# Optimization experiments

Hardware: AMD Instinct MI355X
Metric: run time of the kernel (lower is better)

## Reference

```python
import jax, jax.numpy as jnp
import numpy as np

B, T, S, D, V, PAD = 8, 4095, 2048, 300, 32000, 1


def setup_inputs() -> dict:
    key = jax.random.key(0)
    k1, k2, k3, k4 = jax.random.split(key, 4)
    # tokens in [2, V) so none collide with padding_idx
    x = jax.random.randint(k1, (B, T), 2, V, dtype=jnp.int64)
    # first S nodes are leaves: indices (i, i); remaining T-S are internal spans hi > lo
    leaf = jnp.arange(S, dtype=jnp.int64)
    leaf_pairs = jnp.broadcast_to(jnp.stack([leaf, leaf], -1)[None], (B, S, 2))
    n_int = T - S
    lo = jax.random.randint(k2, (B, n_int), 0, S - 1, dtype=jnp.int64)
    span = jax.random.randint(k3, (B, n_int), 1, 64, dtype=jnp.int64)
    hi = jnp.minimum(lo + span, S - 1)
    int_pairs = jnp.stack([lo, hi], -1)
    indices = jnp.concatenate([leaf_pairs, int_pairs], axis=1)  # [B, T, 2]
    W = jax.random.normal(k4, (V, D), jnp.float32) * 0.02
    W = W.at[PAD].set(0.0)  # padding_idx row is zero, as in nn.Embedding
    return {"x": x, "indices": indices, "W": W}


def reference(x, indices, W):
    b, t = x.shape
    s = (t + 1) // 2
    # _retrieve_leaves: left-pack tokens whose (lo==hi) and token != PAD
    is_leaf = (indices[:, :, 0] == indices[:, :, 1]) & (x != PAD)  # [b,t]
    pos = jnp.cumsum(is_leaf.astype(jnp.int32), axis=1) - 1       # packed slot per leaf
    safe_pos = jnp.where(is_leaf, pos, s)                          # out-of-range -> dropped
    leaves = jnp.full((b, s), PAD, dtype=x.dtype)
    leaves = leaves.at[jnp.arange(b)[:, None], safe_pos].set(x, mode="drop")  # [b,s]
    # interval mask: lo <= r <= hi  (computed as (r>=lo) XOR (r>hi), as in source)
    r = jnp.arange(s)[None, None, :]                               # [1,1,s]
    mask = ((r >= indices[:, :, 0:1]) ^ (r > indices[:, :, 1:2])).astype(W.dtype)  # [b,t,s]
    emb = W[leaves]                                                # [b,s,D]
    denom = jnp.maximum(mask.sum(-1, keepdims=True), 1.0)          # [b,t,1]
    # same math as (mask[...,None] * emb[:,None]).sum(2), without the [b,t,s,D] tensor
    out = jnp.einsum("bts,bsd->btd", mask, emb) / denom
    return out
```

## Files before the change

### kernel.cpp

```cpp
#include <hip/hip_runtime.h>


#define BB 8
#define TT 4095
#define SS 2048
#define DD 300
#define D4 75
#define PADIDX 1
#define CHUNK 16
#define NC (SS / CHUNK)
#define NTB 320

typedef float f4 __attribute__((ext_vector_type(4)));

__global__ __launch_bounds__(NTB) void csumP_kernel(const int* __restrict__ x,
                                                    const float* __restrict__ W,
                                                    float* __restrict__ csum,
                                                    float* __restrict__ P,
                                                    float* __restrict__ out) {
    int blk = blockIdx.x;
    int b = blk & 7, c = blk >> 3;
    int tid = threadIdx.x;
    int g = tid / 80, j = tid - g * 80;
    __shared__ f4 sw[CHUNK][D4];
    const int* xb = x + b * TT + c * CHUNK;
    const f4* W4 = (const f4*)W;
    f4* out4 = (f4*)out;
    if (j < D4) {
#pragma unroll
        for (int i = 0; i < 4; ++i) {
            int row = g * 4 + i;
            f4 v = W4[(size_t)xb[row] * D4 + j];
            sw[row][j] = v;
            __builtin_nontemporal_store(
                v, &out4[((size_t)b * TT + c * CHUNK + row) * D4 + j]);
        }
    }
    __syncthreads();
    if (j >= D4) return;

    f4* P4 = (f4*)P + (size_t)b * (SS + 1) * D4;
    f4 run = (f4)0.f;
    for (int k = 0; k < g * 4; ++k) run += sw[k][j];
    int s0 = c * CHUNK;
#pragma unroll
    for (int i = 0; i < 4; ++i) {
        int row = g * 4 + i;
        P4[(size_t)(s0 + row) * D4 + j] = run;
        run += sw[row][j];
    }
    if (g == 3) {
        ((f4*)csum)[(b * NC + c) * D4 + j] = run;
        if (c == NC - 1) P4[(size_t)SS * D4 + j] = (f4)0.f;
    }
}

__global__ __launch_bounds__(128) void base_kernel(const float* __restrict__ csum,
                                                   float* __restrict__ base) {
    int b = blockIdx.x;
    int j = threadIdx.x;
    if (j >= D4) return;
    const f4* csum4 = (const f4*)csum + (size_t)b * NC * D4;
    f4* base4 = (f4*)base + (size_t)b * (NC + 1) * D4;
    f4 run = (f4)0.f;
#pragma unroll 16
    for (int c = 0; c < NC; ++c) {
        base4[c * D4 + j] = run;
        run += csum4[c * D4 + j];
    }
    base4[NC * D4 + j] = run;
}

__global__ __launch_bounds__(NTB) void out_int_kernel(const int* __restrict__ idx,
                                                      const float* __restrict__ P,
                                                      const float* __restrict__ base,
                                                      float* __restrict__ out) {
    int tid = threadIdx.x;
    int r = tid / 80, j = tid - r * 80;
    int b = blockIdx.x & 7;
    int g = blockIdx.x >> 3;
    const f4* P4 = (const f4*)P + (size_t)b * (SS + 1) * D4;
    const f4* B4 = (const f4*)base + (size_t)b * (NC + 1) * D4;
    f4* out4 = (f4*)out;
    const int2* ixb = (const int2*)(idx + 2 * b * TT);
#pragma unroll
    for (int it = 0; it < 4; ++it) {
        int lr = SS + g * 16 + it * 4 + r;
        if (lr >= TT || j >= D4) continue;
        int2 pr = ixb[lr];
        int u = pr.y + 1;
        int a = min(pr.x, u), e = max(pr.x, u);
        a = max(0, min(a, SS));
        e = max(0, min(e, SS));
        int cnt = e - a;
        float inv = 1.0f / (float)(cnt > 0 ? cnt : 1);
        f4 ve = P4[(size_t)e * D4 + j] + B4[(e >> 4) * D4 + j];
        f4 va = P4[(size_t)a * D4 + j] + B4[(a >> 4) * D4 + j];
        f4 o = (ve - va) * inv;
        __builtin_nontemporal_store(o, &out4[((size_t)b * TT + lr) * D4 + j]);
    }
}

extern "C" void kernel_launch(void* const* d_in, const int* in_sizes, int n_in,
                              void* d_out, int out_size, void* d_ws, size_t ws_size,
                              hipStream_t stream) {
    const int* x = (const int*)d_in[0];
    const int* idx = (const int*)d_in[1];
    const float* W = (const float*)d_in[2];
    float* out = (float*)d_out;

    char* ws = (char*)d_ws;
    float* csum = (float*)ws;
    float* base = (float*)(ws + 1228800);
    float* P = (float*)(ws + 1228800 + 1238400);

    csumP_kernel<<<BB * NC, NTB, 0, stream>>>(x, W, csum, P, out);
    base_kernel<<<BB, 128, 0, stream>>>(csum, base);
    out_int_kernel<<<BB * NC, NTB, 0, stream>>>(idx, P, base, out);
}
```

Measured before the change: 111.1 us.

## Drop chunk-prefix kernel; sum chunk totals directly per interval

Removes the serial base_kernel, which scanned 128 chunk sums per batch using only 8 blocks, along with its launch. Each interval thread now adds the per-chunk totals between the lo and hi chunks itself. Spans are under 64, so this is at most about 4 extra loads per output. It trades a serial, low-occupancy kernel and a launch for a few extra scattered loads per output.

```diff
diff --git a/kernel.cpp b/kernel.cpp
--- a/kernel.cpp
+++ b/kernel.cpp
@@ -55,32 +55,16 @@
     }
 }
 
-__global__ __launch_bounds__(128) void base_kernel(const float* __restrict__ csum,
-                                                   float* __restrict__ base) {
-    int b = blockIdx.x;
-    int j = threadIdx.x;
-    if (j >= D4) return;
-    const f4* csum4 = (const f4*)csum + (size_t)b * NC * D4;
-    f4* base4 = (f4*)base + (size_t)b * (NC + 1) * D4;
-    f4 run = (f4)0.f;
-#pragma unroll 16
-    for (int c = 0; c < NC; ++c) {
-        base4[c * D4 + j] = run;
-        run += csum4[c * D4 + j];
-    }
-    base4[NC * D4 + j] = run;
-}
-
 __global__ __launch_bounds__(NTB) void out_int_kernel(const int* __restrict__ idx,
                                                       const float* __restrict__ P,
-                                                      const float* __restrict__ base,
+                                                      const float* __restrict__ csum,
                                                       float* __restrict__ out) {
     int tid = threadIdx.x;
     int r = tid / 80, j = tid - r * 80;
     int b = blockIdx.x & 7;
     int g = blockIdx.x >> 3;
     const f4* P4 = (const f4*)P + (size_t)b * (SS + 1) * D4;
-    const f4* B4 = (const f4*)base + (size_t)b * (NC + 1) * D4;
+    const f4* C4 = (const f4*)csum + (size_t)b * NC * D4;
     f4* out4 = (f4*)out;
     const int2* ixb = (const int2*)(idx + 2 * b * TT);
 #pragma unroll
@@ -94,9 +78,10 @@
         e = max(0, min(e, SS));
         int cnt = e - a;
         float inv = 1.0f / (float)(cnt > 0 ? cnt : 1);
-        f4 ve = P4[(size_t)e * D4 + j] + B4[(e >> 4) * D4 + j];
-        f4 va = P4[(size_t)a * D4 + j] + B4[(a >> 4) * D4 + j];
-        f4 o = (ve - va) * inv;
+        f4 diff = P4[(size_t)e * D4 + j] - P4[(size_t)a * D4 + j];
+        for (int cc = a >> 4; cc < (e >> 4); ++cc)
+            diff += C4[cc * D4 + j];
+        f4 o = diff * inv;
         __builtin_nontemporal_store(o, &out4[((size_t)b * TT + lr) * D4 + j]);
     }
 }
@@ -111,10 +96,8 @@
 
     char* ws = (char*)d_ws;
     float* csum = (float*)ws;
-    float* base = (float*)(ws + 1228800);
-    float* P = (float*)(ws + 1228800 + 1238400);
+    float* P = (float*)(ws + 1228800);
 
     csumP_kernel<<<BB * NC, NTB, 0, stream>>>(x, W, csum, P, out);
-    base_kernel<<<BB, 128, 0, stream>>>(csum, base);
-    out_int_kernel<<<BB * NC, NTB, 0, stream>>>(idx, P, base, out);
+    out_int_kernel<<<BB * NC, NTB, 0, stream>>>(idx, P, csum, out);
 }
```

Result: faster. 103.7 us (-6.7%).
